# Optimization experiments

Measured on AMD Instinct MI355X. Metric: run time of the kernel, lower is better.

The kernel has to match this reference:

```python
import jax, jax.numpy as jnp
import numpy as np

V, E, D = 100000, 128, 60  # vocab, embedding_size, d_alpha
B, J, M, P = 512, 101, 50, 5120
EPS = 1e-6


def setup_inputs() -> dict:
    key = jax.random.key(0)
    ks = jax.random.split(key, 12)
    s = 0.5 / E
    inp = {
        'batch_titems': jax.random.randint(ks[0], (B, J), 0, V),
        'batch_citems': jax.random.randint(ks[1], (B, M), 0, V),
        'batch_pad_ids': jax.random.randint(ks[2], (2, P), 0, M),
        't_emb': jax.random.uniform(ks[3], (V, E), jnp.float32, -s, s),
        'c_emb': jax.random.uniform(ks[4], (V, E), jnp.float32, -s, s),
        'Ac_w': jax.random.normal(ks[5], (D, E), jnp.float32) * 0.05,
        'Ac_b': jnp.zeros((D,), jnp.float32),
        'At_w': jax.random.normal(ks[6], (D, E), jnp.float32) * 0.05,
        'At_b': jnp.zeros((D,), jnp.float32),
        'Bc_w': jax.random.normal(ks[7], (E, E), jnp.float32) * 0.05,
        'Bc_b': jnp.zeros((E,), jnp.float32),
        'R_w': jax.random.normal(ks[8], (E, E), jnp.float32) * 0.05,
        'R_b': jnp.zeros((E,), jnp.float32),
    }
    return inp


def reference(batch_titems, batch_citems, batch_pad_ids, t_emb, c_emb,
              Ac_w, Ac_b, At_w, At_b, Bc_w, Bc_b, R_w, R_b):
    v = t_emb[batch_titems]            # [B, J, E] target item vectors
    u = c_emb[batch_citems]            # [B, M, E] context item vectors
    tp = v @ At_w.T + At_b             # [B, J, D]
    cp = u @ Ac_w.T + Ac_b             # [B, M, D]
    # cosine similarity with torch eps clamp on norms
    dot = jnp.einsum('bjd,bmd->bjm', tp, cp)
    nt = jnp.maximum(jnp.linalg.norm(tp, axis=-1), EPS)  # [B, J]
    nc = jnp.maximum(jnp.linalg.norm(cp, axis=-1), EPS)  # [B, M]
    cos = dot / (nt[:, :, None] * nc[:, None, :])        # [B, J, M]
    # pad mask: (batch, context-pos) pairs masked across all J target rows
    mask = jnp.zeros((cos.shape[0], cos.shape[2]), bool)
    mask = mask.at[batch_pad_ids[0], batch_pad_ids[1]].set(True)
    scores = jnp.where(mask[:, None, :], -jnp.inf, cos)
    attn = jax.nn.softmax(scores, axis=-1)               # [B, J, M]
    bu = u @ Bc_w.T + Bc_b                               # [B, M, E]
    alpha = jnp.einsum('bjm,bme->bje', attn, bu)         # [B, J, E]
    return alpha @ R_w.T + R_b                           # [B, J, E]
```

## Files before the change

### kernel.cpp

```cpp
#include <hip/hip_runtime.h>

typedef unsigned short u16;
typedef unsigned int   u32;
typedef short bf8 __attribute__((ext_vector_type(8)));
typedef float f4  __attribute__((ext_vector_type(4)));

#define NB   512
#define NJ   101
#define NM   50
#define NE   128
#define ND   60
#define NP   5120
#define NT   512
#define EPSV 1e-6f

#define X_B    0
#define W_B    17408
#define GT_B   34816
#define T_B    52224
#define C_B    68352
#define NTF_B  77568
#define NCF_B  78016
#define BAT_B  78272
#define BAC_B  78528
#define BCB_B  78784
#define RB_B   79296
#define MSK_B  79808
#define TIDX_B 80064
#define ARENA  80512

__device__ __forceinline__ u32 pk2(float a, float b) {
    u32 ia = __float_as_uint(a) + 0x8000u;
    u32 ib = __float_as_uint(b) + 0x8000u;
    return (ia >> 16) | (ib & 0xFFFF0000u);
}
__device__ __forceinline__ u16 f2bh(float f) {
    return (u16)((__float_as_uint(f) + 0x8000u) >> 16);
}
__device__ __forceinline__ bf8 gfrag(const float* p) {
    const float4* q = (const float4*)p;
    float4 x = q[0], y = q[1];
    union { u32 u[4]; bf8 v; } r;
    r.u[0] = pk2(x.x, x.y); r.u[1] = pk2(x.z, x.w);
    r.u[2] = pk2(y.x, y.y); r.u[3] = pk2(y.z, y.w);
    return r.v;
}

__global__ __launch_bounds__(NT, 4) void aitv_kernel(
    const int* __restrict__ titems, const int* __restrict__ citems,
    const int* __restrict__ pad_ids,
    const float* __restrict__ t_emb, const float* __restrict__ c_emb,
    const float* __restrict__ Ac_w,  const float* __restrict__ Ac_b,
    const float* __restrict__ At_w,  const float* __restrict__ At_b,
    const float* __restrict__ Bc_w,  const float* __restrict__ Bc_b,
    const float* __restrict__ R_w,   const float* __restrict__ R_b,
    float* __restrict__ out)
{
    const int b    = blockIdx.x;
    const int t    = threadIdx.x;
    const int wid  = t >> 6;
    const int lane = t & 63;
    const int l15  = lane & 15;
    const int quad = lane >> 4;

    __shared__ __align__(16) char arena[ARENA];
    u16*   us16 = (u16*)(arena + X_B);   u32* us32 = (u32*)(arena + X_B);
    u16*   ws16 = (u16*)(arena + W_B);   u32* ws32 = (u32*)(arena + W_B);
    float* Wf   = (float*)(arena + W_B);
    u16*   buW  = (u16*)(arena + W_B);
    u16*   gT16 = (u16*)(arena + GT_B);
    u16*   tp16 = (u16*)(arena + T_B);   u32* tpu32 = (u32*)(arena + T_B);
    u16*   at16 = (u16*)(arena + T_B);
    u16*   cp16 = (u16*)(arena + C_B);   u32* cpu32 = (u32*)(arena + C_B);
    float* ntf  = (float*)(arena + NTF_B);
    float* ncf  = (float*)(arena + NCF_B);
    float* bat  = (float*)(arena + BAT_B);
    float* bac  = (float*)(arena + BAC_B);
    float* bcb  = (float*)(arena + BCB_B);
    float* rb   = (float*)(arena + RB_B);
    int*   msk  = (int*)(arena + MSK_B);
    int*   tidx = (int*)(arena + TIDX_B);

    for (int i = t; i < 64 * 64; i += NT) {
        int row = i >> 6, c2 = i & 63;
        u32 val = 0;
        if (row < NM) {
            int idx = citems[b * NM + row];
            float2 x = *(const float2*)(c_emb + (size_t)idx * NE + 2 * c2);
            val = pk2(x.x, x.y);
        }
        us32[row * 68 + c2] = val;
    }
    for (int i = t; i < 128 * 64; i += NT) {
        int row = i >> 6, c2 = i & 63;
        u32 val = 0;
        if (row < ND) {
            float2 x = *(const float2*)(At_w + row * NE + 2 * c2);
            val = pk2(x.x, x.y);
        } else if (row >= 64 && row < 64 + ND) {
            float2 x = *(const float2*)(Ac_w + (row - 64) * NE + 2 * c2);
            val = pk2(x.x, x.y);
        }
        ws32[row * 68 + c2] = val;
    }
    if (t < 64) {
        msk[t] = 0;
        bat[t] = (t < ND) ? At_b[t] : 0.f;
        bac[t] = (t < ND) ? Ac_b[t] : 0.f;
    } else if (t >= 128 && t < 256) {
        int i = t - 128;
        bcb[i] = Bc_b[i];
        rb[i]  = R_b[i];
    } else if (t >= 256 && t < 368) {
        int i = t - 256;
        tidx[i] = titems[b * NJ + ((i < NJ) ? i : (NJ - 1))];
    }
    __syncthreads();

    for (int i = t; i < NP; i += NT)
        if (pad_ids[i] == b) msk[pad_ids[NP + i]] = 1;

    for (int u = wid; u < 44; u += 8) {
        if (u < 28) {
            int jt = u >> 2, dt = u & 3;
            const float* vrow = t_emb + (size_t)tidx[jt * 16 + l15] * NE;
            float bv = bat[dt * 16 + l15];
            f4 acc = {bv, bv, bv, bv};
            #pragma unroll
            for (int ks = 0; ks < 4; ks++) {
                bf8 a  = gfrag(vrow + ks * 32 + quad * 8);
                bf8 bb = *(const bf8*)(ws16 + (dt * 16 + l15) * 136 + ks * 32 + quad * 8);
                acc = __builtin_amdgcn_mfma_f32_16x16x32_bf16(a, bb, acc, 0, 0, 0);
            }
            int d = dt * 16 + l15, j0 = jt * 16 + quad * 4;
            for (int r = 0; r < 4; r++) tp16[(j0 + r) * 72 + d] = f2bh(acc[r]);
        } else {
            int uu = u - 28, mt = uu >> 2, dt = uu & 3;
            float bv = bac[dt * 16 + l15];
            f4 acc = {bv, bv, bv, bv};
            #pragma unroll
            for (int ks = 0; ks < 4; ks++) {
                bf8 a  = *(const bf8*)(us16 + (mt * 16 + l15) * 136 + ks * 32 + quad * 8);
                bf8 bb = *(const bf8*)(ws16 + (64 + dt * 16 + l15) * 136 + ks * 32 + quad * 8);
                acc = __builtin_amdgcn_mfma_f32_16x16x32_bf16(a, bb, acc, 0, 0, 0);
            }
            int d = dt * 16 + l15, m0 = mt * 16 + quad * 4;
            for (int r = 0; r < 4; r++) cp16[(m0 + r) * 72 + d] = f2bh(acc[r]);
        }
    }
    __syncthreads();

    if (t < 112) {
        float s = 0.f;
        for (int c2 = 0; c2 < 32; c2++) {
            u32 w = tpu32[t * 36 + c2];
            union { u32 i; float f; } x, y; x.i = w << 16; y.i = w & 0xFFFF0000u;
            s += x.f * x.f + y.f * y.f;
        }
        ntf[t] = fmaxf(sqrtf(s), EPSV);
    } else if (t < 176) {
        int r = t - 112;
        float s = 0.f;
        for (int c2 = 0; c2 < 32; c2++) {
            u32 w = cpu32[r * 36 + c2];
            union { u32 i; float f; } x, y; x.i = w << 16; y.i = w & 0xFFFF0000u;
            s += x.f * x.f + y.f * y.f;
        }
        ncf[r] = fmaxf(sqrtf(s), EPSV);
    }
    for (int u = wid; u < 28; u += 8) {
        int jt = u >> 2, mt = u & 3;
        f4 acc = {0.f, 0.f, 0.f, 0.f};
        #pragma unroll
        for (int ks = 0; ks < 2; ks++) {
            bf8 a  = *(const bf8*)(tp16 + (jt * 16 + l15) * 72 + ks * 32 + quad * 8);
            bf8 bb = *(const bf8*)(cp16 + (mt * 16 + l15) * 72 + ks * 32 + quad * 8);
            acc = __builtin_amdgcn_mfma_f32_16x16x32_bf16(a, bb, acc, 0, 0, 0);
        }
        int m = mt * 16 + l15, j0 = jt * 16 + quad * 4;
        for (int r = 0; r < 4; r++) Wf[(j0 + r) * 68 + m] = acc[r];
    }
    __syncthreads();

    for (int j = wid; j < 112; j += 8) {
        float sc = -INFINITY;
        if (lane < NM && msk[lane] == 0)
            sc = Wf[j * 68 + lane] / (ntf[j] * ncf[lane]);
        float mx = sc;
        for (int o = 32; o; o >>= 1) mx = fmaxf(mx, __shfl_xor(mx, o, 64));
        float p = (mx > -INFINITY) ? __expf(sc - mx) : 0.f;
        float sm = p;
        for (int o = 32; o; o >>= 1) sm += __shfl_xor(sm, o, 64);
        float inv = (sm > 0.f) ? 1.f / sm : 0.f;
        at16[j * 72 + lane] = (lane < NM) ? f2bh(p * inv) : (u16)0;
    }
    __syncthreads();

    for (int u = wid; u < 32; u += 8) {
        int mt = u >> 3, et = u & 7;
        const float* brow = Bc_w + (size_t)(et * 16 + l15) * NE;
        float bv = bcb[et * 16 + l15];
        f4 acc = {bv, bv, bv, bv};
        #pragma unroll
        for (int ks = 0; ks < 4; ks++) {
            bf8 a  = *(const bf8*)(us16 + (mt * 16 + l15) * 136 + ks * 32 + quad * 8);
            bf8 bb = gfrag(brow + ks * 32 + quad * 8);
            acc = __builtin_amdgcn_mfma_f32_16x16x32_bf16(a, bb, acc, 0, 0, 0);
        }
        int e = et * 16 + l15, m0 = mt * 16 + quad * 4;
        for (int r = 0; r < 4; r++) buW[(m0 + r) * 136 + e] = f2bh(acc[r]);
    }
    __syncthreads();

    for (int u = wid; u < 32; u += 8) {
        int et = u >> 2, mt = u & 3;
        const float* arow = R_w + (size_t)(et * 16 + l15) * NE;
        f4 acc = {0.f, 0.f, 0.f, 0.f};
        #pragma unroll
        for (int ks = 0; ks < 4; ks++) {
            bf8 a  = gfrag(arow + ks * 32 + quad * 8);
            bf8 bb = *(const bf8*)(buW + (mt * 16 + l15) * 136 + ks * 32 + quad * 8);
            acc = __builtin_amdgcn_mfma_f32_16x16x32_bf16(a, bb, acc, 0, 0, 0);
        }
        int m = mt * 16 + l15, e0 = et * 16 + quad * 4;
        for (int r = 0; r < 4; r++) gT16[(e0 + r) * 68 + m] = f2bh(acc[r]);
    }
    __syncthreads();

    for (int u = wid; u < 56; u += 8) {
        int jt = u >> 3, et = u & 7;
        float bv = rb[et * 16 + l15];
        f4 acc = {bv, bv, bv, bv};
        #pragma unroll
        for (int ks = 0; ks < 2; ks++) {
            bf8 a  = *(const bf8*)(at16 + (jt * 16 + l15) * 72 + ks * 32 + quad * 8);
            bf8 bb = *(const bf8*)(gT16 + (et * 16 + l15) * 68 + ks * 32 + quad * 8);
            acc = __builtin_amdgcn_mfma_f32_16x16x32_bf16(a, bb, acc, 0, 0, 0);
        }
        int e = et * 16 + l15, j0 = jt * 16 + quad * 4;
        for (int r = 0; r < 4; r++) {
            int j = j0 + r;
            if (j < NJ) out[((size_t)b * NJ + j) * NE + e] = acc[r];
        }
    }
}

extern "C" void kernel_launch(void* const* d_in, const int* in_sizes, int n_in,
                              void* d_out, int out_size, void* d_ws, size_t ws_size,
                              hipStream_t stream) {
    const int*   titems  = (const int*)d_in[0];
    const int*   citems  = (const int*)d_in[1];
    const int*   pad_ids = (const int*)d_in[2];
    const float* t_emb   = (const float*)d_in[3];
    const float* c_emb   = (const float*)d_in[4];
    const float* Ac_w    = (const float*)d_in[5];
    const float* Ac_b    = (const float*)d_in[6];
    const float* At_w    = (const float*)d_in[7];
    const float* At_b    = (const float*)d_in[8];
    const float* Bc_w    = (const float*)d_in[9];
    const float* Bc_b    = (const float*)d_in[10];
    const float* R_w     = (const float*)d_in[11];
    const float* R_b     = (const float*)d_in[12];
    float* out = (float*)d_out;

    aitv_kernel<<<NB, NT, 0, stream>>>(titems, citems, pad_ids, t_emb, c_emb,
                                       Ac_w, Ac_b, At_w, At_b, Bc_w, Bc_b,
                                       R_w, R_b, out);
}
```

Measured before the change: 203.8 us.

## Precompute fused R·Bc weight, fuse norms into projections and softmax into scores

Adds a small pre-kernel that folds the R and Bc linear layers into one 128x128 bf16 weight plus a combined bias, so each block does one fewer GEMM stage. Norms are now accumulated through shuffle reductions and LDS atomics inside the projection epilogue, and the score GEMM computes the cosine softmax directly in registers, which removes the separate norm and softmax passes and their barriers. Projection weights are read straight from global memory instead of being staged in LDS, which shrinks shared memory and may raise occupancy. The cost is an extra kernel launch and different bf16 rounding from the fused weight product.

```diff
diff --git a/kernel.cpp b/kernel.cpp
--- a/kernel.cpp
+++ b/kernel.cpp
@@ -14,28 +14,26 @@
 #define NT   512
 #define EPSV 1e-6f
 
-#define X_B    0
-#define W_B    17408
-#define GT_B   34816
-#define T_B    52224
-#define C_B    68352
-#define NTF_B  77568
-#define NCF_B  78016
-#define BAT_B  78272
-#define BAC_B  78528
-#define BCB_B  78784
-#define RB_B   79296
-#define MSK_B  79808
-#define TIDX_B 80064
-#define ARENA  80512
-
+#define U_B    0
+#define T_B    17408
+#define C_B    33536
+#define H_B    42752
+#define NT2_B  61184
+#define NC2_B  61632
+#define BAT_B  61888
+#define BAC_B  62144
+#define RB2_B  62400
+#define MSK_B  62912
+#define TIDX_B 63168
+#define ARENA  63616
+
+__device__ __forceinline__ u16 f2bh(float f) {
+    return (u16)((__float_as_uint(f) + 0x8000u) >> 16);
+}
 __device__ __forceinline__ u32 pk2(float a, float b) {
     u32 ia = __float_as_uint(a) + 0x8000u;
     u32 ib = __float_as_uint(b) + 0x8000u;
     return (ia >> 16) | (ib & 0xFFFF0000u);
-}
-__device__ __forceinline__ u16 f2bh(float f) {
-    return (u16)((__float_as_uint(f) + 0x8000u) >> 16);
 }
 __device__ __forceinline__ bf8 gfrag(const float* p) {
     const float4* q = (const float4*)p;
@@ -46,14 +44,32 @@
     return r.v;
 }
 
+__global__ __launch_bounds__(128) void w2_kernel(
+    const float* __restrict__ Bc_w, const float* __restrict__ Bc_b,
+    const float* __restrict__ R_w,  const float* __restrict__ R_b,
+    u16* __restrict__ w2t, float* __restrict__ rb2)
+{
+    const int e = blockIdx.x, k = threadIdx.x;
+    const float* Rrow = R_w + e * NE;
+    float acc = 0.f;
+    #pragma unroll 8
+    for (int j = 0; j < NE; j++) acc += Rrow[j] * Bc_w[j * NE + k];
+    w2t[e * NE + k] = f2bh(acc);
+    float c = Bc_b[k] * Rrow[k];
+    for (int o = 32; o; o >>= 1) c += __shfl_xor(c, o, 64);
+    __shared__ float part[2];
+    if ((k & 63) == 0) part[k >> 6] = c;
+    __syncthreads();
+    if (k == 0) rb2[e] = part[0] + part[1] + R_b[e];
+}
+
 __global__ __launch_bounds__(NT, 4) void aitv_kernel(
     const int* __restrict__ titems, const int* __restrict__ citems,
     const int* __restrict__ pad_ids,
     const float* __restrict__ t_emb, const float* __restrict__ c_emb,
     const float* __restrict__ Ac_w,  const float* __restrict__ Ac_b,
     const float* __restrict__ At_w,  const float* __restrict__ At_b,
-    const float* __restrict__ Bc_w,  const float* __restrict__ Bc_b,
-    const float* __restrict__ R_w,   const float* __restrict__ R_b,
+    const u16* __restrict__ w2t,     const float* __restrict__ rb2g,
     float* __restrict__ out)
 {
     const int b    = blockIdx.x;
@@ -64,20 +80,15 @@
     const int quad = lane >> 4;
 
     __shared__ __align__(16) char arena[ARENA];
-    u16*   us16 = (u16*)(arena + X_B);   u32* us32 = (u32*)(arena + X_B);
-    u16*   ws16 = (u16*)(arena + W_B);   u32* ws32 = (u32*)(arena + W_B);
-    float* Wf   = (float*)(arena + W_B);
-    u16*   buW  = (u16*)(arena + W_B);
-    u16*   gT16 = (u16*)(arena + GT_B);
-    u16*   tp16 = (u16*)(arena + T_B);   u32* tpu32 = (u32*)(arena + T_B);
-    u16*   at16 = (u16*)(arena + T_B);
-    u16*   cp16 = (u16*)(arena + C_B);   u32* cpu32 = (u32*)(arena + C_B);
-    float* ntf  = (float*)(arena + NTF_B);
-    float* ncf  = (float*)(arena + NCF_B);
+    u16*   us16 = (u16*)(arena + U_B);   u32* us32 = (u32*)(arena + U_B);
+    u16*   tp16 = (u16*)(arena + T_B);   u16* at16 = (u16*)(arena + T_B);
+    u16*   cp16 = (u16*)(arena + C_B);
+    u16*   hT16 = (u16*)(arena + H_B);
+    float* nt2  = (float*)(arena + NT2_B);
+    float* nc2  = (float*)(arena + NC2_B);
     float* bat  = (float*)(arena + BAT_B);
     float* bac  = (float*)(arena + BAC_B);
-    float* bcb  = (float*)(arena + BCB_B);
-    float* rb   = (float*)(arena + RB_B);
+    float* rb2  = (float*)(arena + RB2_B);
     int*   msk  = (int*)(arena + MSK_B);
     int*   tidx = (int*)(arena + TIDX_B);
 
@@ -91,150 +102,139 @@
         }
         us32[row * 68 + c2] = val;
     }
-    for (int i = t; i < 128 * 64; i += NT) {
-        int row = i >> 6, c2 = i & 63;
-        u32 val = 0;
-        if (row < ND) {
-            float2 x = *(const float2*)(At_w + row * NE + 2 * c2);
-            val = pk2(x.x, x.y);
-        } else if (row >= 64 && row < 64 + ND) {
-            float2 x = *(const float2*)(Ac_w + (row - 64) * NE + 2 * c2);
-            val = pk2(x.x, x.y);
-        }
-        ws32[row * 68 + c2] = val;
-    }
-    if (t < 64) {
-        msk[t] = 0;
-        bat[t] = (t < ND) ? At_b[t] : 0.f;
-        bac[t] = (t < ND) ? Ac_b[t] : 0.f;
-    } else if (t >= 128 && t < 256) {
-        int i = t - 128;
-        bcb[i] = Bc_b[i];
-        rb[i]  = R_b[i];
-    } else if (t >= 256 && t < 368) {
-        int i = t - 256;
-        tidx[i] = titems[b * NJ + ((i < NJ) ? i : (NJ - 1))];
-    }
+    if (t < 112) { nt2[t] = 0.f; tidx[t] = titems[b * NJ + ((t < NJ) ? t : NJ - 1)]; }
+    if (t >= 128 && t < 192) { int i = t - 128; nc2[i] = 0.f; msk[i] = 0; }
+    if (t >= 192 && t < 256) {
+        int i = t - 192;
+        bat[i] = (i < ND) ? At_b[i] : 0.f;
+        bac[i] = (i < ND) ? Ac_b[i] : 0.f;
+    }
+    if (t >= 256 && t < 384) rb2[t - 256] = rb2g[t - 256];
     __syncthreads();
 
     for (int i = t; i < NP; i += NT)
         if (pad_ids[i] == b) msk[pad_ids[NP + i]] = 1;
 
-    for (int u = wid; u < 44; u += 8) {
+    for (int u = wid; u < 76; u += 8) {
         if (u < 28) {
             int jt = u >> 2, dt = u & 3;
+            int d  = dt * 16 + l15;
             const float* vrow = t_emb + (size_t)tidx[jt * 16 + l15] * NE;
-            float bv = bat[dt * 16 + l15];
+            const float* arow = At_w + (size_t)((d < ND) ? d : ND - 1) * NE;
+            float bv = bat[d];
             f4 acc = {bv, bv, bv, bv};
             #pragma unroll
             for (int ks = 0; ks < 4; ks++) {
                 bf8 a  = gfrag(vrow + ks * 32 + quad * 8);
-                bf8 bb = *(const bf8*)(ws16 + (dt * 16 + l15) * 136 + ks * 32 + quad * 8);
-                acc = __builtin_amdgcn_mfma_f32_16x16x32_bf16(a, bb, acc, 0, 0, 0);
-            }
-            int d = dt * 16 + l15, j0 = jt * 16 + quad * 4;
-            for (int r = 0; r < 4; r++) tp16[(j0 + r) * 72 + d] = f2bh(acc[r]);
-        } else {
+                bf8 bb = gfrag(arow + ks * 32 + quad * 8);
+                acc = __builtin_amdgcn_mfma_f32_16x16x32_bf16(a, bb, acc, 0, 0, 0);
+            }
+            int j0 = jt * 16 + quad * 4;
+            #pragma unroll
+            for (int r = 0; r < 4; r++) {
+                float v = acc[r];
+                tp16[(j0 + r) * 72 + d] = (d < ND) ? f2bh(v) : (u16)0;
+                float q = (d < ND) ? v * v : 0.f;
+                q += __shfl_xor(q, 1, 64); q += __shfl_xor(q, 2, 64);
+                q += __shfl_xor(q, 4, 64); q += __shfl_xor(q, 8, 64);
+                if (l15 == 0) atomicAdd(&nt2[j0 + r], q);
+            }
+        } else if (u < 44) {
             int uu = u - 28, mt = uu >> 2, dt = uu & 3;
-            float bv = bac[dt * 16 + l15];
+            int d = dt * 16 + l15;
+            const float* arow = Ac_w + (size_t)((d < ND) ? d : ND - 1) * NE;
+            float bv = bac[d];
             f4 acc = {bv, bv, bv, bv};
             #pragma unroll
             for (int ks = 0; ks < 4; ks++) {
                 bf8 a  = *(const bf8*)(us16 + (mt * 16 + l15) * 136 + ks * 32 + quad * 8);
-                bf8 bb = *(const bf8*)(ws16 + (64 + dt * 16 + l15) * 136 + ks * 32 + quad * 8);
-                acc = __builtin_amdgcn_mfma_f32_16x16x32_bf16(a, bb, acc, 0, 0, 0);
-            }
-            int d = dt * 16 + l15, m0 = mt * 16 + quad * 4;
-            for (int r = 0; r < 4; r++) cp16[(m0 + r) * 72 + d] = f2bh(acc[r]);
-        }
-    }
-    __syncthreads();
-
-    if (t < 112) {
-        float s = 0.f;
-        for (int c2 = 0; c2 < 32; c2++) {
-            u32 w = tpu32[t * 36 + c2];
-            union { u32 i; float f; } x, y; x.i = w << 16; y.i = w & 0xFFFF0000u;
-            s += x.f * x.f + y.f * y.f;
-        }
-        ntf[t] = fmaxf(sqrtf(s), EPSV);
-    } else if (t < 176) {
-        int r = t - 112;
-        float s = 0.f;
-        for (int c2 = 0; c2 < 32; c2++) {
-            u32 w = cpu32[r * 36 + c2];
-            union { u32 i; float f; } x, y; x.i = w << 16; y.i = w & 0xFFFF0000u;
-            s += x.f * x.f + y.f * y.f;
-        }
-        ncf[r] = fmaxf(sqrtf(s), EPSV);
-    }
-    for (int u = wid; u < 28; u += 8) {
-        int jt = u >> 2, mt = u & 3;
-        f4 acc = {0.f, 0.f, 0.f, 0.f};
-        #pragma unroll
-        for (int ks = 0; ks < 2; ks++) {
-            bf8 a  = *(const bf8*)(tp16 + (jt * 16 + l15) * 72 + ks * 32 + quad * 8);
-            bf8 bb = *(const bf8*)(cp16 + (mt * 16 + l15) * 72 + ks * 32 + quad * 8);
-            acc = __builtin_amdgcn_mfma_f32_16x16x32_bf16(a, bb, acc, 0, 0, 0);
-        }
-        int m = mt * 16 + l15, j0 = jt * 16 + quad * 4;
-        for (int r = 0; r < 4; r++) Wf[(j0 + r) * 68 + m] = acc[r];
-    }
-    __syncthreads();
-
-    for (int j = wid; j < 112; j += 8) {
-        float sc = -INFINITY;
-        if (lane < NM && msk[lane] == 0)
-            sc = Wf[j * 68 + lane] / (ntf[j] * ncf[lane]);
-        float mx = sc;
-        for (int o = 32; o; o >>= 1) mx = fmaxf(mx, __shfl_xor(mx, o, 64));
-        float p = (mx > -INFINITY) ? __expf(sc - mx) : 0.f;
-        float sm = p;
-        for (int o = 32; o; o >>= 1) sm += __shfl_xor(sm, o, 64);
-        float inv = (sm > 0.f) ? 1.f / sm : 0.f;
-        at16[j * 72 + lane] = (lane < NM) ? f2bh(p * inv) : (u16)0;
-    }
-    __syncthreads();
-
-    for (int u = wid; u < 32; u += 8) {
-        int mt = u >> 3, et = u & 7;
-        const float* brow = Bc_w + (size_t)(et * 16 + l15) * NE;
-        float bv = bcb[et * 16 + l15];
-        f4 acc = {bv, bv, bv, bv};
-        #pragma unroll
-        for (int ks = 0; ks < 4; ks++) {
-            bf8 a  = *(const bf8*)(us16 + (mt * 16 + l15) * 136 + ks * 32 + quad * 8);
-            bf8 bb = gfrag(brow + ks * 32 + quad * 8);
-            acc = __builtin_amdgcn_mfma_f32_16x16x32_bf16(a, bb, acc, 0, 0, 0);
-        }
-        int e = et * 16 + l15, m0 = mt * 16 + quad * 4;
-        for (int r = 0; r < 4; r++) buW[(m0 + r) * 136 + e] = f2bh(acc[r]);
-    }
-    __syncthreads();
-
-    for (int u = wid; u < 32; u += 8) {
-        int et = u >> 2, mt = u & 3;
-        const float* arow = R_w + (size_t)(et * 16 + l15) * NE;
-        f4 acc = {0.f, 0.f, 0.f, 0.f};
-        #pragma unroll
-        for (int ks = 0; ks < 4; ks++) {
-            bf8 a  = gfrag(arow + ks * 32 + quad * 8);
-            bf8 bb = *(const bf8*)(buW + (mt * 16 + l15) * 136 + ks * 32 + quad * 8);
-            acc = __builtin_amdgcn_mfma_f32_16x16x32_bf16(a, bb, acc, 0, 0, 0);
-        }
-        int m = mt * 16 + l15, e0 = et * 16 + quad * 4;
-        for (int r = 0; r < 4; r++) gT16[(e0 + r) * 68 + m] = f2bh(acc[r]);
+                bf8 bb = gfrag(arow + ks * 32 + quad * 8);
+                acc = __builtin_amdgcn_mfma_f32_16x16x32_bf16(a, bb, acc, 0, 0, 0);
+            }
+            int m0 = mt * 16 + quad * 4;
+            #pragma unroll
+            for (int r = 0; r < 4; r++) {
+                float v = acc[r];
+                cp16[(m0 + r) * 72 + d] = (d < ND) ? f2bh(v) : (u16)0;
+                float q = (d < ND) ? v * v : 0.f;
+                q += __shfl_xor(q, 1, 64); q += __shfl_xor(q, 2, 64);
+                q += __shfl_xor(q, 4, 64); q += __shfl_xor(q, 8, 64);
+                if (l15 == 0) atomicAdd(&nc2[m0 + r], q);
+            }
+        } else {
+            int uu = u - 44, et = uu >> 2, mt = uu & 3;
+            const u16* arow = w2t + (size_t)(et * 16 + l15) * NE;
+            f4 acc = {0.f, 0.f, 0.f, 0.f};
+            #pragma unroll
+            for (int ks = 0; ks < 4; ks++) {
+                bf8 a  = *(const bf8*)(arow + ks * 32 + quad * 8);
+                bf8 bb = *(const bf8*)(us16 + (mt * 16 + l15) * 136 + ks * 32 + quad * 8);
+                acc = __builtin_amdgcn_mfma_f32_16x16x32_bf16(a, bb, acc, 0, 0, 0);
+            }
+            int e0 = et * 16 + quad * 4;
+            for (int r = 0; r < 4; r++)
+                hT16[(e0 + r) * 72 + mt * 16 + l15] = f2bh(acc[r]);
+        }
+    }
+    __syncthreads();
+
+    if (wid < 7) {
+        const int jt = wid;
+        f4 S[4];
+        #pragma unroll
+        for (int mt = 0; mt < 4; mt++) {
+            f4 acc = {0.f, 0.f, 0.f, 0.f};
+            #pragma unroll
+            for (int ks = 0; ks < 2; ks++) {
+                bf8 a  = *(const bf8*)(tp16 + (jt * 16 + l15) * 72 + ks * 32 + quad * 8);
+                bf8 bb = *(const bf8*)(cp16 + (mt * 16 + l15) * 72 + ks * 32 + quad * 8);
+                acc = __builtin_amdgcn_mfma_f32_16x16x32_bf16(a, bb, acc, 0, 0, 0);
+            }
+            S[mt] = acc;
+        }
+        bool  valid[4]; float ncS[4];
+        #pragma unroll
+        for (int mt = 0; mt < 4; mt++) {
+            int m = mt * 16 + l15;
+            valid[mt] = (m < NM) && (msk[m] == 0);
+            ncS[mt]   = valid[mt] ? fmaxf(sqrtf(nc2[m]), EPSV) : 1.f;
+        }
+        #pragma unroll
+        for (int r = 0; r < 4; r++) {
+            int j = jt * 16 + quad * 4 + r;
+            float ntj = fmaxf(sqrtf(nt2[j]), EPSV);
+            float x[4], mx = -INFINITY;
+            #pragma unroll
+            for (int mt = 0; mt < 4; mt++) {
+                x[mt] = valid[mt] ? S[mt][r] / (ntj * ncS[mt]) : -INFINITY;
+                mx = fmaxf(mx, x[mt]);
+            }
+            mx = fmaxf(mx, __shfl_xor(mx, 1, 64)); mx = fmaxf(mx, __shfl_xor(mx, 2, 64));
+            mx = fmaxf(mx, __shfl_xor(mx, 4, 64)); mx = fmaxf(mx, __shfl_xor(mx, 8, 64));
+            float p[4], sm = 0.f;
+            #pragma unroll
+            for (int mt = 0; mt < 4; mt++) {
+                p[mt] = valid[mt] ? __expf(x[mt] - mx) : 0.f;
+                sm += p[mt];
+            }
+            sm += __shfl_xor(sm, 1, 64); sm += __shfl_xor(sm, 2, 64);
+            sm += __shfl_xor(sm, 4, 64); sm += __shfl_xor(sm, 8, 64);
+            float inv = (sm > 0.f) ? 1.f / sm : 0.f;
+            #pragma unroll
+            for (int mt = 0; mt < 4; mt++)
+                at16[j * 72 + mt * 16 + l15] = f2bh(p[mt] * inv);
+        }
     }
     __syncthreads();
 
     for (int u = wid; u < 56; u += 8) {
         int jt = u >> 3, et = u & 7;
-        float bv = rb[et * 16 + l15];
+        float bv = rb2[et * 16 + l15];
         f4 acc = {bv, bv, bv, bv};
         #pragma unroll
         for (int ks = 0; ks < 2; ks++) {
             bf8 a  = *(const bf8*)(at16 + (jt * 16 + l15) * 72 + ks * 32 + quad * 8);
-            bf8 bb = *(const bf8*)(gT16 + (et * 16 + l15) * 68 + ks * 32 + quad * 8);
+            bf8 bb = *(const bf8*)(hT16 + (et * 16 + l15) * 72 + ks * 32 + quad * 8);
             acc = __builtin_amdgcn_mfma_f32_16x16x32_bf16(a, bb, acc, 0, 0, 0);
         }
         int e = et * 16 + l15, j0 = jt * 16 + quad * 4;
@@ -263,7 +263,10 @@
     const float* R_b     = (const float*)d_in[12];
     float* out = (float*)d_out;
 
+    u16*   w2t = (u16*)d_ws;
+    float* rb2 = (float*)((char*)d_ws + 32768);
+
+    w2_kernel<<<NE, NE, 0, stream>>>(Bc_w, Bc_b, R_w, R_b, w2t, rb2);
     aitv_kernel<<<NB, NT, 0, stream>>>(titems, citems, pad_ids, t_emb, c_emb,
-                                       Ac_w, Ac_b, At_w, At_b, Bc_w, Bc_b,
-                                       R_w, R_b, out);
-}
+                                       Ac_w, Ac_b, At_w, At_b, w2t, rb2, out);
+}
```

Result: faster. 190.9 us (-6.3%).
